# Optimization experiments

Measured on AMD Instinct MI355X. Metric: run time of the kernel, lower is better.

Reference implementation:

```python
import jax, jax.numpy as jnp
import numpy as np

B, R, H, F = 65536, 64, 10, 5


def setup_inputs() -> dict:
    key = jax.random.key(0)
    ks = jax.random.split(key, 14)
    return {
        "r_emb": jax.random.normal(ks[0], (B, R, H), jnp.float32),
        "feature": jax.random.normal(ks[1], (B, F), jnp.float32),
        "h0": jax.random.normal(ks[2], (B, H), jnp.float32),
        "c0": jax.random.normal(ks[3], (B, H), jnp.float32),
        "W_ih": jax.random.normal(ks[4], (4 * H, H), jnp.float32) * 0.3,
        "W_hh": jax.random.normal(ks[5], (4 * H, H), jnp.float32) * 0.3,
        "b_ih": jax.random.normal(ks[6], (4 * H,), jnp.float32) * 0.1,
        "b_hh": jax.random.normal(ks[7], (4 * H,), jnp.float32) * 0.1,
        "Wr": jax.random.normal(ks[8], (H, H), jnp.float32) * 0.3,
        "br": jax.random.normal(ks[9], (H,), jnp.float32) * 0.1,
        "Wh": jax.random.normal(ks[10], (H, H), jnp.float32) * 0.3,
        "bh": jax.random.normal(ks[11], (H,), jnp.float32) * 0.1,
        "Wfc": jax.random.normal(ks[12], (1, R * H + F), jnp.float32) * 0.1,
        "bfc": jax.random.normal(ks[13], (1,), jnp.float32) * 0.1,
    }


def reference(r_emb, feature, h0, c0, W_ih, W_hh, b_ih, b_hh, Wr, br, Wh, bh, Wfc, bfc):
    # r_emb: [B, R, H] -> scan over regions (time-major [R, B, H])
    xs = jnp.swapaxes(r_emb, 0, 1)

    def step(carry, x_t):
        h, c = carry
        # PyTorch LSTMCell gate order: i, f, g, o
        gates = x_t @ W_ih.T + b_ih + h @ W_hh.T + b_hh  # [B, 4H]
        i, f, g, o = jnp.split(gates, 4, axis=-1)
        c_new = jax.nn.sigmoid(f) * c + jax.nn.sigmoid(i) * jnp.tanh(g)
        h_new = jax.nn.sigmoid(o) * jnp.tanh(c_new)
        gate = jax.nn.sigmoid(x_t @ Wr.T + br + h_new @ Wh.T + bh)
        return (h_new, c_new), h_new * gate

    (_, _), outs = jax.lax.scan(step, (h0, c0), xs)  # outs: [R, B, H]
    flat = jnp.swapaxes(outs, 0, 1).reshape(r_emb.shape[0], -1)  # [B, R*H]
    fc_in = jnp.concatenate([flat, feature], axis=1)  # [B, R*H + F]
    return fc_in @ Wfc.T + bfc  # [B, 1]
```

## Files before the change

kernel.cpp:

```cpp
#include <hip/hip_runtime.h>

#define Rn 64
#define Hn 10
#define Fn 5
#define XRS 52

typedef float f32x2 __attribute__((ext_vector_type(2)));
typedef float f32x4 __attribute__((ext_vector_type(4)));

#define PKFMA(a, b, c) __builtin_elementwise_fma((a), (b), (c))

__device__ __forceinline__ float fsigmoid(float x) {
    return __builtin_amdgcn_rcpf(1.0f + __expf(-x));
}
__device__ __forceinline__ float ftanh(float x) {
    return 1.0f - 2.0f * __builtin_amdgcn_rcpf(__expf(2.0f * x) + 1.0f);
}

__global__ __launch_bounds__(256, 2) void seqreader_kernel(
    const float* __restrict__ r_emb,
    const float* __restrict__ feature,
    const float* __restrict__ h0,
    const float* __restrict__ c0,
    const float* __restrict__ W_ih,
    const float* __restrict__ W_hh,
    const float* __restrict__ b_ih,
    const float* __restrict__ b_hh,
    const float* __restrict__ Wr,
    const float* __restrict__ br,
    const float* __restrict__ Wh,
    const float* __restrict__ bh,
    const float* __restrict__ Wfc,
    const float* __restrict__ bfc,
    float* __restrict__ out)
{
    __shared__ __align__(16) float sWih[40 * 12];
    __shared__ __align__(16) float sWhh[40 * 12];
    __shared__ __align__(16) float sWr[10 * 12];
    __shared__ __align__(16) float sWhn[10 * 12];
    __shared__ float sWfc[646];
    __shared__ __align__(16) float sX[2][128 * XRS];

    const int tid  = threadIdx.x;
    const int lane = tid & 63;
    const int half = lane >> 5;
    const int r0h  = half * 5;
    const int bb   = (tid >> 6) * 32 + (lane & 31);
    const int b0   = blockIdx.x * 128;
    const int b    = b0 + bb;

    for (int i = tid; i < 400; i += 256) {
        int r = i / 10, k = i - r * 10;
        sWih[r * 12 + k] = W_ih[i];
        sWhh[r * 12 + k] = W_hh[i];
    }
    for (int i = tid; i < 100; i += 256) {
        int r = i / 10, k = i - r * 10;
        sWr[r * 12 + k]  = Wr[i];
        sWhn[r * 12 + k] = Wh[i];
    }
    for (int i = tid; i < 645; i += 256) sWfc[i] = Wfc[i];

    float bi[5], bf_[5], bg_[5], bo[5], brh[5];
#pragma unroll
    for (int j = 0; j < 5; ++j) {
        bi[j]  = b_ih[0  + r0h + j] + b_hh[0  + r0h + j];
        bf_[j] = b_ih[10 + r0h + j] + b_hh[10 + r0h + j];
        bg_[j] = b_ih[20 + r0h + j] + b_hh[20 + r0h + j];
        bo[j]  = b_ih[30 + r0h + j] + b_hh[30 + r0h + j];
        brh[j] = br[r0h + j] + bh[r0h + j];
    }

    float c[5];
#pragma unroll
    for (int j = 0; j < 5; ++j) c[j] = c0[b * Hn + r0h + j];
    float hf[Hn];
#pragma unroll
    for (int k = 0; k < Hn; ++k) hf[k] = h0[b * Hn + k];

    float acc = 0.0f;
    if (half == 0) {
        acc = bfc[0];
#pragma unroll
        for (int k = 0; k < Fn; ++k)
            acc = fmaf(feature[b * Fn + k], Wfc[Rn * Hn + k], acc);
    }

    unsigned off_g[5], off_l[5][4];
#pragma unroll
    for (int k = 0; k < 5; ++k) {
        int q  = k * 256 + tid;
        int bq = q / 10;
        int e  = q - bq * 10;
        off_g[k] = (unsigned)((bq * (Rn * Hn) + e * 4) * 4);
#pragma unroll
        for (int cidx = 0; cidx < 4; ++cidx) {
            int u = e * 4 + cidx;
            int s = u / 10, kk = u - s * 10;
            off_l[k][cidx] = (unsigned)(bq * XRS + s * 12 + kk);
        }
    }
    const char* gb = (const char*)(r_emb + (size_t)b0 * (Rn * Hn));

    {
        float4 s0[5];
#pragma unroll
        for (int k = 0; k < 5; ++k) s0[k] = *(const float4*)(gb + off_g[k]);
#pragma unroll
        for (int k = 0; k < 5; ++k) {
            sX[0][off_l[k][0]] = s0[k].x;
            sX[0][off_l[k][1]] = s0[k].y;
            sX[0][off_l[k][2]] = s0[k].z;
            sX[0][off_l[k][3]] = s0[k].w;
        }
    }
    __syncthreads();

    float4 st[5];
#pragma unroll 1
    for (int t = 0; t < Rn; ++t) {
        const int tt = t & 3;
        const int Tb = (t >> 2) & 1;

        if (tt == 0 && t + 4 < Rn) {
#pragma unroll
            for (int k = 0; k < 5; ++k)
                st[k] = *(const float4*)(gb + off_g[k] + (unsigned)(t / 4 + 1) * 160u);
        }

        const f32x4* xr = (const f32x4*)&sX[Tb][bb * XRS + tt * 12];
        const f32x4 xq0 = xr[0], xq1 = xr[1], xq2 = xr[2];
        const f32x2 x01 = xq0.lo, x23 = xq0.hi, x45 = xq1.lo, x67 = xq1.hi, x89 = xq2.lo;

        f32x2 h2[5];
#pragma unroll
        for (int p = 0; p < 5; ++p) h2[p] = f32x2{hf[2 * p], hf[2 * p + 1]};

        float hn[5];
#pragma unroll
        for (int j = 0; j < 5; ++j) {
            float zg[4];
#pragma unroll
            for (int gidx = 0; gidx < 4; ++gidx) {
                const int row = gidx * 10 + r0h + j;
                const f32x4* wi = (const f32x4*)&sWih[row * 12];
                const f32x4* wh = (const f32x4*)&sWhh[row * 12];
                const f32x4 wi0 = wi[0], wi1 = wi[1], wi2 = wi[2];
                const f32x4 wh0 = wh[0], wh1 = wh[1], wh2 = wh[2];
                f32x2 z2 = {0.f, 0.f};
                z2 = PKFMA(wi0.lo, x01, z2);
                z2 = PKFMA(wi0.hi, x23, z2);
                z2 = PKFMA(wi1.lo, x45, z2);
                z2 = PKFMA(wi1.hi, x67, z2);
                z2 = PKFMA(wi2.lo, x89, z2);
                z2 = PKFMA(wh0.lo, h2[0], z2);
                z2 = PKFMA(wh0.hi, h2[1], z2);
                z2 = PKFMA(wh1.lo, h2[2], z2);
                z2 = PKFMA(wh1.hi, h2[3], z2);
                z2 = PKFMA(wh2.lo, h2[4], z2);
                zg[gidx] = z2[0] + z2[1];
            }
            const float si = fsigmoid(zg[0] + bi[j]);
            const float sf = fsigmoid(zg[1] + bf_[j]);
            const float tg = ftanh(zg[2] + bg_[j]);
            const float so = fsigmoid(zg[3] + bo[j]);
            const float cn = fmaf(sf, c[j], si * tg);
            c[j] = cn;
            hn[j] = so * ftanh(cn);
        }

        float sw[5];
#pragma unroll
        for (int j = 0; j < 5; ++j) sw[j] = __shfl_xor(hn[j], 32, 64);
#pragma unroll
        for (int j = 0; j < 5; ++j) {
            hf[j]     = half ? sw[j] : hn[j];
            hf[5 + j] = half ? hn[j] : sw[j];
        }

        if (tt == 2 && t + 2 < Rn) {
#pragma unroll
            for (int k = 0; k < 5; ++k) {
                sX[Tb ^ 1][off_l[k][0]] = st[k].x;
                sX[Tb ^ 1][off_l[k][1]] = st[k].y;
                sX[Tb ^ 1][off_l[k][2]] = st[k].z;
                sX[Tb ^ 1][off_l[k][3]] = st[k].w;
            }
        }

        f32x2 hn2[5];
#pragma unroll
        for (int p = 0; p < 5; ++p) hn2[p] = f32x2{hf[2 * p], hf[2 * p + 1]};
#pragma unroll
        for (int j = 0; j < 5; ++j) {
            const int row = r0h + j;
            const f32x4* wr_ = (const f32x4*)&sWr[row * 12];
            const f32x4* wh_ = (const f32x4*)&sWhn[row * 12];
            const f32x4 wr0 = wr_[0], wr1 = wr_[1], wr2 = wr_[2];
            const f32x4 wh0 = wh_[0], wh1 = wh_[1], wh2 = wh_[2];
            f32x2 z2 = {0.f, 0.f};
            z2 = PKFMA(wr0.lo, x01, z2);
            z2 = PKFMA(wr0.hi, x23, z2);
            z2 = PKFMA(wr1.lo, x45, z2);
            z2 = PKFMA(wr1.hi, x67, z2);
            z2 = PKFMA(wr2.lo, x89, z2);
            z2 = PKFMA(wh0.lo, hn2[0], z2);
            z2 = PKFMA(wh0.hi, hn2[1], z2);
            z2 = PKFMA(wh1.lo, hn2[2], z2);
            z2 = PKFMA(wh1.hi, hn2[3], z2);
            z2 = PKFMA(wh2.lo, hn2[4], z2);
            const float s = z2[0] + z2[1] + brh[j];
            acc = fmaf(hn[j] * fsigmoid(s), sWfc[t * Hn + r0h + j], acc);
        }

        if (tt == 3) __syncthreads();
    }

    acc += __shfl_xor(acc, 32, 64);
    if (half == 0) out[b] = acc;
}

extern "C" void kernel_launch(void* const* d_in, const int* in_sizes, int n_in,
                              void* d_out, int out_size, void* d_ws, size_t ws_size,
                              hipStream_t stream) {
    const float* r_emb   = (const float*)d_in[0];
    const float* feature = (const float*)d_in[1];
    const float* h0      = (const float*)d_in[2];
    const float* c0      = (const float*)d_in[3];
    const float* W_ih    = (const float*)d_in[4];
    const float* W_hh    = (const float*)d_in[5];
    const float* b_ih    = (const float*)d_in[6];
    const float* b_hh    = (const float*)d_in[7];
    const float* Wr      = (const float*)d_in[8];
    const float* br      = (const float*)d_in[9];
    const float* Wh      = (const float*)d_in[10];
    const float* bh      = (const float*)d_in[11];
    const float* Wfc     = (const float*)d_in[12];
    const float* bfc     = (const float*)d_in[13];
    float* out = (float*)d_out;

    dim3 grid(65536 / 128), block(256);
    hipLaunchKernelGGL(seqreader_kernel, grid, block, 0, stream,
                       r_emb, feature, h0, c0, W_ih, W_hh, b_ih, b_hh,
                       Wr, br, Wh, bh, Wfc, bfc, out);
}
```

Measured before the change: 211.5 us.

## Process two batch rows per thread to reuse LDS weight loads

Each thread now carries two independent LSTM sequences (rows b and b+128), so every weight vector read from LDS feeds two packed-FMA chains. The block covers 256 batch rows, the grid is halved, and the shared staging buffer and prefetch registers are doubled. The aim is to cut LDS weight traffic per FMA and add instruction-level parallelism. In exchange register pressure roughly doubles (launch bounds relaxed to 1 block), only 256 blocks are launched, and occupancy drops, which could hurt latency hiding.

```diff
diff --git a/kernel.cpp b/kernel.cpp
--- a/kernel.cpp
+++ b/kernel.cpp
@@ -17,7 +17,7 @@
     return 1.0f - 2.0f * __builtin_amdgcn_rcpf(__expf(2.0f * x) + 1.0f);
 }
 
-__global__ __launch_bounds__(256, 2) void seqreader_kernel(
+__global__ __launch_bounds__(256, 1) void seqreader_kernel(
     const float* __restrict__ r_emb,
     const float* __restrict__ feature,
     const float* __restrict__ h0,
@@ -39,15 +39,16 @@
     __shared__ __align__(16) float sWr[10 * 12];
     __shared__ __align__(16) float sWhn[10 * 12];
     __shared__ float sWfc[646];
-    __shared__ __align__(16) float sX[2][128 * XRS];
+    __shared__ __align__(16) float sX[2][256 * XRS];
 
     const int tid  = threadIdx.x;
     const int lane = tid & 63;
     const int half = lane >> 5;
     const int r0h  = half * 5;
     const int bb   = (tid >> 6) * 32 + (lane & 31);
-    const int b0   = blockIdx.x * 128;
-    const int b    = b0 + bb;
+    const int b0   = blockIdx.x * 256;
+    const int bA   = b0 + bb;
+    const int bB   = b0 + bb + 128;
 
     for (int i = tid; i < 400; i += 256) {
         int r = i / 10, k = i - r * 10;
@@ -71,24 +72,33 @@
         brh[j] = br[r0h + j] + bh[r0h + j];
     }
 
-    float c[5];
-#pragma unroll
-    for (int j = 0; j < 5; ++j) c[j] = c0[b * Hn + r0h + j];
-    float hf[Hn];
-#pragma unroll
-    for (int k = 0; k < Hn; ++k) hf[k] = h0[b * Hn + k];
-
-    float acc = 0.0f;
+    float cA[5], cB[5];
+#pragma unroll
+    for (int j = 0; j < 5; ++j) {
+        cA[j] = c0[(size_t)bA * Hn + r0h + j];
+        cB[j] = c0[(size_t)bB * Hn + r0h + j];
+    }
+    float hfA[Hn], hfB[Hn];
+#pragma unroll
+    for (int k = 0; k < Hn; ++k) {
+        hfA[k] = h0[(size_t)bA * Hn + k];
+        hfB[k] = h0[(size_t)bB * Hn + k];
+    }
+
+    float accA = 0.0f, accB = 0.0f;
     if (half == 0) {
-        acc = bfc[0];
-#pragma unroll
-        for (int k = 0; k < Fn; ++k)
-            acc = fmaf(feature[b * Fn + k], Wfc[Rn * Hn + k], acc);
-    }
-
-    unsigned off_g[5], off_l[5][4];
-#pragma unroll
-    for (int k = 0; k < 5; ++k) {
+        accA = bfc[0];
+        accB = bfc[0];
+#pragma unroll
+        for (int k = 0; k < Fn; ++k) {
+            accA = fmaf(feature[(size_t)bA * Fn + k], Wfc[Rn * Hn + k], accA);
+            accB = fmaf(feature[(size_t)bB * Fn + k], Wfc[Rn * Hn + k], accB);
+        }
+    }
+
+    unsigned off_g[10], off_l[10][4];
+#pragma unroll
+    for (int k = 0; k < 10; ++k) {
         int q  = k * 256 + tid;
         int bq = q / 10;
         int e  = q - bq * 10;
@@ -103,11 +113,11 @@
     const char* gb = (const char*)(r_emb + (size_t)b0 * (Rn * Hn));
 
     {
-        float4 s0[5];
-#pragma unroll
-        for (int k = 0; k < 5; ++k) s0[k] = *(const float4*)(gb + off_g[k]);
-#pragma unroll
-        for (int k = 0; k < 5; ++k) {
+        float4 s0[10];
+#pragma unroll
+        for (int k = 0; k < 10; ++k) s0[k] = *(const float4*)(gb + off_g[k]);
+#pragma unroll
+        for (int k = 0; k < 10; ++k) {
             sX[0][off_l[k][0]] = s0[k].x;
             sX[0][off_l[k][1]] = s0[k].y;
             sX[0][off_l[k][2]] = s0[k].z;
@@ -116,7 +126,7 @@
     }
     __syncthreads();
 
-    float4 st[5];
+    float4 st[10];
 #pragma unroll 1
     for (int t = 0; t < Rn; ++t) {
         const int tt = t & 3;
@@ -124,22 +134,26 @@
 
         if (tt == 0 && t + 4 < Rn) {
 #pragma unroll
-            for (int k = 0; k < 5; ++k)
+            for (int k = 0; k < 10; ++k)
                 st[k] = *(const float4*)(gb + off_g[k] + (unsigned)(t / 4 + 1) * 160u);
         }
 
-        const f32x4* xr = (const f32x4*)&sX[Tb][bb * XRS + tt * 12];
-        const f32x4 xq0 = xr[0], xq1 = xr[1], xq2 = xr[2];
-        const f32x2 x01 = xq0.lo, x23 = xq0.hi, x45 = xq1.lo, x67 = xq1.hi, x89 = xq2.lo;
-
-        f32x2 h2[5];
-#pragma unroll
-        for (int p = 0; p < 5; ++p) h2[p] = f32x2{hf[2 * p], hf[2 * p + 1]};
-
-        float hn[5];
+        const f32x4* xrA = (const f32x4*)&sX[Tb][bb * XRS + tt * 12];
+        const f32x4* xrB = (const f32x4*)&sX[Tb][(bb + 128) * XRS + tt * 12];
+        const f32x4 xa0 = xrA[0], xa1 = xrA[1], xa2 = xrA[2];
+        const f32x4 xb0 = xrB[0], xb1 = xrB[1], xb2 = xrB[2];
+
+        f32x2 hA[5], hB[5];
+#pragma unroll
+        for (int p = 0; p < 5; ++p) {
+            hA[p] = f32x2{hfA[2 * p], hfA[2 * p + 1]};
+            hB[p] = f32x2{hfB[2 * p], hfB[2 * p + 1]};
+        }
+
+        float hnA[5], hnB[5];
 #pragma unroll
         for (int j = 0; j < 5; ++j) {
-            float zg[4];
+            float zgA[4], zgB[4];
 #pragma unroll
             for (int gidx = 0; gidx < 4; ++gidx) {
                 const int row = gidx * 10 + r0h + j;
@@ -147,40 +161,53 @@
                 const f32x4* wh = (const f32x4*)&sWhh[row * 12];
                 const f32x4 wi0 = wi[0], wi1 = wi[1], wi2 = wi[2];
                 const f32x4 wh0 = wh[0], wh1 = wh[1], wh2 = wh[2];
-                f32x2 z2 = {0.f, 0.f};
-                z2 = PKFMA(wi0.lo, x01, z2);
-                z2 = PKFMA(wi0.hi, x23, z2);
-                z2 = PKFMA(wi1.lo, x45, z2);
-                z2 = PKFMA(wi1.hi, x67, z2);
-                z2 = PKFMA(wi2.lo, x89, z2);
-                z2 = PKFMA(wh0.lo, h2[0], z2);
-                z2 = PKFMA(wh0.hi, h2[1], z2);
-                z2 = PKFMA(wh1.lo, h2[2], z2);
-                z2 = PKFMA(wh1.hi, h2[3], z2);
-                z2 = PKFMA(wh2.lo, h2[4], z2);
-                zg[gidx] = z2[0] + z2[1];
-            }
-            const float si = fsigmoid(zg[0] + bi[j]);
-            const float sf = fsigmoid(zg[1] + bf_[j]);
-            const float tg = ftanh(zg[2] + bg_[j]);
-            const float so = fsigmoid(zg[3] + bo[j]);
-            const float cn = fmaf(sf, c[j], si * tg);
-            c[j] = cn;
-            hn[j] = so * ftanh(cn);
-        }
-
-        float sw[5];
-#pragma unroll
-        for (int j = 0; j < 5; ++j) sw[j] = __shfl_xor(hn[j], 32, 64);
+                f32x2 zA = {0.f, 0.f}, zB = {0.f, 0.f};
+                zA = PKFMA(wi0.lo, xa0.lo, zA);  zB = PKFMA(wi0.lo, xb0.lo, zB);
+                zA = PKFMA(wi0.hi, xa0.hi, zA);  zB = PKFMA(wi0.hi, xb0.hi, zB);
+                zA = PKFMA(wi1.lo, xa1.lo, zA);  zB = PKFMA(wi1.lo, xb1.lo, zB);
+                zA = PKFMA(wi1.hi, xa1.hi, zA);  zB = PKFMA(wi1.hi, xb1.hi, zB);
+                zA = PKFMA(wi2.lo, xa2.lo, zA);  zB = PKFMA(wi2.lo, xb2.lo, zB);
+                zA = PKFMA(wh0.lo, hA[0], zA);   zB = PKFMA(wh0.lo, hB[0], zB);
+                zA = PKFMA(wh0.hi, hA[1], zA);   zB = PKFMA(wh0.hi, hB[1], zB);
+                zA = PKFMA(wh1.lo, hA[2], zA);   zB = PKFMA(wh1.lo, hB[2], zB);
+                zA = PKFMA(wh1.hi, hA[3], zA);   zB = PKFMA(wh1.hi, hB[3], zB);
+                zA = PKFMA(wh2.lo, hA[4], zA);   zB = PKFMA(wh2.lo, hB[4], zB);
+                zgA[gidx] = zA[0] + zA[1];
+                zgB[gidx] = zB[0] + zB[1];
+            }
+            {
+                const float si = fsigmoid(zgA[0] + bi[j]);
+                const float sf = fsigmoid(zgA[1] + bf_[j]);
+                const float tg = ftanh(zgA[2] + bg_[j]);
+                const float so = fsigmoid(zgA[3] + bo[j]);
+                const float cn = fmaf(sf, cA[j], si * tg);
+                cA[j] = cn;
+                hnA[j] = so * ftanh(cn);
+            }
+            {
+                const float si = fsigmoid(zgB[0] + bi[j]);
+                const float sf = fsigmoid(zgB[1] + bf_[j]);
+                const float tg = ftanh(zgB[2] + bg_[j]);
+                const float so = fsigmoid(zgB[3] + bo[j]);
+                const float cn = fmaf(sf, cB[j], si * tg);
+                cB[j] = cn;
+                hnB[j] = so * ftanh(cn);
+            }
+        }
+
 #pragma unroll
         for (int j = 0; j < 5; ++j) {
-            hf[j]     = half ? sw[j] : hn[j];
-            hf[5 + j] = half ? hn[j] : sw[j];
+            const float swA = __shfl_xor(hnA[j], 32, 64);
+            const float swB = __shfl_xor(hnB[j], 32, 64);
+            hfA[j]     = half ? swA : hnA[j];
+            hfA[5 + j] = half ? hnA[j] : swA;
+            hfB[j]     = half ? swB : hnB[j];
+            hfB[5 + j] = half ? hnB[j] : swB;
         }
 
         if (tt == 2 && t + 2 < Rn) {
 #pragma unroll
-            for (int k = 0; k < 5; ++k) {
+            for (int k = 0; k < 10; ++k) {
                 sX[Tb ^ 1][off_l[k][0]] = st[k].x;
                 sX[Tb ^ 1][off_l[k][1]] = st[k].y;
                 sX[Tb ^ 1][off_l[k][2]] = st[k].z;
@@ -188,9 +215,12 @@
             }
         }
 
-        f32x2 hn2[5];
-#pragma unroll
-        for (int p = 0; p < 5; ++p) hn2[p] = f32x2{hf[2 * p], hf[2 * p + 1]};
+        f32x2 hnA2[5], hnB2[5];
+#pragma unroll
+        for (int p = 0; p < 5; ++p) {
+            hnA2[p] = f32x2{hfA[2 * p], hfA[2 * p + 1]};
+            hnB2[p] = f32x2{hfB[2 * p], hfB[2 * p + 1]};
+        }
 #pragma unroll
         for (int j = 0; j < 5; ++j) {
             const int row = r0h + j;
@@ -198,26 +228,33 @@
             const f32x4* wh_ = (const f32x4*)&sWhn[row * 12];
             const f32x4 wr0 = wr_[0], wr1 = wr_[1], wr2 = wr_[2];
             const f32x4 wh0 = wh_[0], wh1 = wh_[1], wh2 = wh_[2];
-            f32x2 z2 = {0.f, 0.f};
-            z2 = PKFMA(wr0.lo, x01, z2);
-            z2 = PKFMA(wr0.hi, x23, z2);
-            z2 = PKFMA(wr1.lo, x45, z2);
-            z2 = PKFMA(wr1.hi, x67, z2);
-            z2 = PKFMA(wr2.lo, x89, z2);
-            z2 = PKFMA(wh0.lo, hn2[0], z2);
-            z2 = PKFMA(wh0.hi, hn2[1], z2);
-            z2 = PKFMA(wh1.lo, hn2[2], z2);
-            z2 = PKFMA(wh1.hi, hn2[3], z2);
-            z2 = PKFMA(wh2.lo, hn2[4], z2);
-            const float s = z2[0] + z2[1] + brh[j];
-            acc = fmaf(hn[j] * fsigmoid(s), sWfc[t * Hn + r0h + j], acc);
+            f32x2 zA = {0.f, 0.f}, zB = {0.f, 0.f};
+            zA = PKFMA(wr0.lo, xa0.lo, zA);  zB = PKFMA(wr0.lo, xb0.lo, zB);
+            zA = PKFMA(wr0.hi, xa0.hi, zA);  zB = PKFMA(wr0.hi, xb0.hi, zB);
+            zA = PKFMA(wr1.lo, xa1.lo, zA);  zB = PKFMA(wr1.lo, xb1.lo, zB);
+            zA = PKFMA(wr1.hi, xa1.hi, zA);  zB = PKFMA(wr1.hi, xb1.hi, zB);
+            zA = PKFMA(wr2.lo, xa2.lo, zA);  zB = PKFMA(wr2.lo, xb2.lo, zB);
+            zA = PKFMA(wh0.lo, hnA2[0], zA); zB = PKFMA(wh0.lo, hnB2[0], zB);
+            zA = PKFMA(wh0.hi, hnA2[1], zA); zB = PKFMA(wh0.hi, hnB2[1], zB);
+            zA = PKFMA(wh1.lo, hnA2[2], zA); zB = PKFMA(wh1.lo, hnB2[2], zB);
+            zA = PKFMA(wh1.hi, hnA2[3], zA); zB = PKFMA(wh1.hi, hnB2[3], zB);
+            zA = PKFMA(wh2.lo, hnA2[4], zA); zB = PKFMA(wh2.lo, hnB2[4], zB);
+            const float sA = zA[0] + zA[1] + brh[j];
+            const float sB = zB[0] + zB[1] + brh[j];
+            const float wf = sWfc[t * Hn + r0h + j];
+            accA = fmaf(hnA[j] * fsigmoid(sA), wf, accA);
+            accB = fmaf(hnB[j] * fsigmoid(sB), wf, accB);
         }
 
         if (tt == 3) __syncthreads();
     }
 
-    acc += __shfl_xor(acc, 32, 64);
-    if (half == 0) out[b] = acc;
+    accA += __shfl_xor(accA, 32, 64);
+    accB += __shfl_xor(accB, 32, 64);
+    if (half == 0) {
+        out[bA] = accA;
+        out[bB] = accB;
+    }
 }
 
 extern "C" void kernel_launch(void* const* d_in, const int* in_sizes, int n_in,
@@ -239,7 +276,7 @@
     const float* bfc     = (const float*)d_in[13];
     float* out = (float*)d_out;
 
-    dim3 grid(65536 / 128), block(256);
+    dim3 grid(65536 / 256), block(256);
     hipLaunchKernelGGL(seqreader_kernel, grid, block, 0, stream,
                        r_emb, feature, h0, c0, W_ih, W_hh, b_ih, b_hh,
                        Wr, br, Wh, bh, Wfc, bfc, out);
```

New measurement: 212.9 us. About the same (+0.6%).
